# Kernel tuning notes

Measured on AMD Instinct MI355X. Metric: run time of the kernel, lower is better.

Reference implementation:

```python
import jax, jax.numpy as jnp
import numpy as np

N = 50000      # nodes
E = 800000     # edges (before self loops)
IN = 128       # in_channels
HID = 64       # hidden_channels
HEADS = 4      # num_heads
OUT = 40       # out_channels
NEG_SLOPE = 0.2


def setup_inputs() -> dict:
    key = jax.random.key(0)
    ks = jax.random.split(key, 16)
    x = jax.random.normal(ks[0], (N, IN), dtype=jnp.float32)
    edge_index = jax.random.randint(ks[1], (2, E), 0, N, dtype=jnp.int64)

    def lin(k, fan_in, fan_out):
        return jax.random.normal(k, (fan_in, fan_out), dtype=jnp.float32) * (1.0 / np.sqrt(fan_in))

    def att(k, h, c):
        return jax.random.normal(k, (h, c), dtype=jnp.float32) * (1.0 / np.sqrt(c))

    return {
        "x": x, "edge_index": edge_index,
        "W1": lin(ks[2], IN, HEADS * HID),
        "as1": att(ks[3], HEADS, HID), "ad1": att(ks[4], HEADS, HID),
        "b1": jnp.zeros((HEADS * HID,), jnp.float32),
        "W2": lin(ks[5], HEADS * HID, HEADS * HID),
        "as2": att(ks[6], HEADS, HID), "ad2": att(ks[7], HEADS, HID),
        "b2": jnp.zeros((HEADS * HID,), jnp.float32),
        "W3": lin(ks[8], HEADS * HID, OUT),
        "as3": att(ks[9], 1, OUT), "ad3": att(ks[10], 1, OUT),
        "b3": jnp.zeros((OUT,), jnp.float32),
    }


def _gat_layer(x, src, dst, W, a_src, a_dst, b):
    """One GATConv: linear -> per-edge attention -> segment softmax -> scatter-sum."""
    n = x.shape[0]
    H, C = a_src.shape
    h = (x @ W).reshape(n, H, C)                       # [N,H,C]
    al_s = jnp.einsum('nhc,hc->nh', h, a_src)          # [N,H]
    al_d = jnp.einsum('nhc,hc->nh', h, a_dst)          # [N,H]
    alpha = jax.nn.leaky_relu(al_s[src] + al_d[dst], NEG_SLOPE)  # [Etot,H]
    m = jax.ops.segment_max(alpha, dst, num_segments=n)          # stable softmax over incoming edges
    e = jnp.exp(alpha - m[dst])
    denom = jax.ops.segment_sum(e, dst, num_segments=n)
    attn = e / denom[dst]                              # [Etot,H]
    out = jax.ops.segment_sum(h[src] * attn[:, :, None], dst, num_segments=n)  # [N,H,C]
    return out.reshape(n, H * C) + b


def reference(x, edge_index, W1, as1, ad1, b1, W2, as2, ad2, b2, W3, as3, ad3, b3):
    # add self loops once (PyG GATConv default add_self_loops=True)
    loops = jnp.arange(N, dtype=edge_index.dtype)
    src = jnp.concatenate([edge_index[0], loops])
    dst = jnp.concatenate([edge_index[1], loops])

    h = _gat_layer(x, src, dst, W1, as1, ad1, b1)
    h = jax.nn.relu(h)                                 # dropout is identity in eval mode
    h = _gat_layer(h, src, dst, W2, as2, ad2, b2)
    h = jax.nn.relu(h)
    h = _gat_layer(h, src, dst, W3, as3, ad3, b3)      # final layer: 1 head
    return jax.nn.log_softmax(h, axis=-1)
```

## Files before the change

### kernel.cpp

```cpp
#include <hip/hip_runtime.h>
#include <math.h>

#define N_NODES 50000
#define N_EDGES 800000
#define ETOT    (N_EDGES + N_NODES)
#define EPAD_MAX 1200000
#define IN_CH   128
#define OUT_CH  40
#define NEG     0.2f
#define CAP     64

#define NPF   98
#define NFINE 512
#define FCAP  2400

typedef __attribute__((ext_vector_type(8))) short bf16x8;
typedef __attribute__((ext_vector_type(4))) float f32x4;
typedef __attribute__((ext_vector_type(2))) float f32x2;

__device__ inline unsigned short f2bf(float f) {
    unsigned int u = __float_as_uint(f);
    return (unsigned short)((u + 0x7FFFu + ((u >> 16) & 1u)) >> 16);
}
__device__ inline float bf2f(unsigned short u) {
    return __uint_as_float((unsigned int)u << 16);
}
__device__ inline float lrelu(float a) { return (a > 0.f) ? a : NEG * a; }

__global__ __launch_bounds__(256) void k_bkt(const int* __restrict__ ei,
                                             int* __restrict__ fcur,
                                             unsigned int* __restrict__ fbuf,
                                             const float* __restrict__ W1,
                                             const float* __restrict__ W2,
                                             const float* __restrict__ W3,
                                             unsigned short* __restrict__ Wt1,
                                             unsigned short* __restrict__ Wt2,
                                             unsigned short* __restrict__ Wt3) {
    if (blockIdx.x >= 256) {
        int i = (blockIdx.x - 256) * 256 + threadIdx.x;
        if (i < 32768) {
            int n = i >> 7, k = i & 127;
            Wt1[i] = f2bf(W1[(long)k * 256 + n]);
        } else if (i < 98304) {
            int j = i - 32768;
            int n = j >> 8, k = j & 255;
            Wt2[j] = f2bf(W2[(long)k * 256 + n]);
        } else if (i < 114688) {
            int j = i - 98304;
            int n = j >> 8, k = j & 255;
            Wt3[j] = (n < OUT_CH) ? f2bf(W3[(long)k * OUT_CH + n]) : (unsigned short)0;
        }
        return;
    }
    __shared__ int lcnt[NFINE], lbase[NFINE], lcur[NFINE];
    int tid = threadIdx.x;
    for (int i = tid; i < NFINE; i += 256) lcnt[i] = 0;
    __syncthreads();
    for (int i = blockIdx.x * 256 + tid; i < ETOT; i += 256 * 256) {
        int d = (i < N_EDGES) ? ei[N_EDGES + i] : (i - N_EDGES);
        atomicAdd(&lcnt[d / NPF], 1);
    }
    __syncthreads();
    for (int i = tid; i < NFINE; i += 256) {
        lbase[i] = atomicAdd(&fcur[i], lcnt[i]);
        lcur[i] = 0;
    }
    __syncthreads();
    for (int i = blockIdx.x * 256 + tid; i < ETOT; i += 256 * 256) {
        int s, d;
        if (i < N_EDGES) { s = ei[i]; d = ei[N_EDGES + i]; }
        else             { s = i - N_EDGES; d = s; }
        int p = d / NPF;
        int off = atomicAdd(&lcur[p], 1);
        fbuf[(long)p * FCAP + lbase[p] + off] = (unsigned int)s | ((unsigned int)d << 16);
    }
}

__global__ __launch_bounds__(256) void k_deg(const int* __restrict__ fcur,
                                             const unsigned int* __restrict__ fbuf,
                                             int* __restrict__ deg,
                                             int* __restrict__ psum) {
    __shared__ int cnt[NPF];
    __shared__ int tot;
    int f = blockIdx.x;
    int tid = threadIdx.x;
    int n0 = f * NPF;
    int nend = min(n0 + NPF, N_NODES);
    int nn = nend - n0;
    if (tid < NPF) cnt[tid] = 0;
    if (tid == 0) tot = 0;
    __syncthreads();
    int n = fcur[f];
    for (int i = tid; i < n; i += 256)
        atomicAdd(&cnt[(int)(fbuf[(long)f * FCAP + i] >> 16) - n0], 1);
    __syncthreads();
    if (tid < NPF && tid < nn) {
        deg[n0 + tid] = cnt[tid];
        atomicAdd(&tot, (cnt[tid] + 7) & ~7);
    }
    __syncthreads();
    if (tid == 0) psum[f] = tot;
}

__global__ __launch_bounds__(512) void k_pscan(int* __restrict__ psum) {
    __shared__ int sh[NFINE];
    int tid = threadIdx.x;
    int v = psum[tid];
    int x = v;
    sh[tid] = x;
    __syncthreads();
    #pragma unroll
    for (int off = 1; off < NFINE; off <<= 1) {
        int t = (tid >= off) ? sh[tid - off] : 0;
        __syncthreads();
        x += t;
        sh[tid] = x;
        __syncthreads();
    }
    psum[tid] = x - v;
}

__global__ __launch_bounds__(256) void k_scat(const int* __restrict__ fcur,
                                              const unsigned int* __restrict__ fbuf,
                                              const int* __restrict__ deg,
                                              const int* __restrict__ psum,
                                              int* __restrict__ start,
                                              int* __restrict__ eSrc) {
    __shared__ int sval[128];
    __shared__ int offs[NPF];
    __shared__ int base[NPF];
    int f = blockIdx.x;
    int tid = threadIdx.x;
    int n0 = f * NPF;
    int nend = min(n0 + NPF, N_NODES);
    int nn = nend - n0;
    int pbase = psum[f];

    int pd = 0;
    if (tid < 128) {
        pd = (tid < nn) ? ((deg[n0 + tid] + 7) & ~7) : 0;
        sval[tid] = pd;
    }
    __syncthreads();
    #pragma unroll
    for (int off = 1; off < 128; off <<= 1) {
        int t = 0;
        if (tid < 128 && tid >= off) t = sval[tid - off];
        __syncthreads();
        if (tid < 128) sval[tid] += t;
        __syncthreads();
    }
    if (tid < 128 && tid < nn) {
        int st = pbase + sval[tid] - pd;
        start[n0 + tid] = st;
        offs[tid] = st;
        base[tid] = st;
    }
    __syncthreads();

    int n = fcur[f];
    for (int i = tid; i < n; i += 256) {
        unsigned int u = fbuf[(long)f * FCAP + i];
        int d = (int)(u >> 16);
        int pos = atomicAdd(&offs[d - n0], 1);
        eSrc[pos] = (int)(u & 0xFFFFu);
    }
    __syncthreads();
    if (tid < NPF && tid < nn) {
        int endp = offs[tid];
        int dg = endp - base[tid];
        int stop = base[tid] + ((dg + 7) & ~7);
        for (int k2 = endp; k2 < stop; ++k2) eSrc[k2] = -1;
    }
}

#define PITCH 40
template<int BN, int FM, int FN, bool CVT, bool FP8OUT, bool L4>
__global__ __launch_bounds__(256) void k_mfma(const void* __restrict__ Araw,
                                              const unsigned short* __restrict__ Bt,
                                              void* __restrict__ Cout,
                                              const float* __restrict__ a_s,
                                              const float* __restrict__ a_d,
                                              float* __restrict__ als,
                                              float* __restrict__ ald,
                                              int M, int K, int Ncol) {
    __shared__ unsigned short As[128 * PITCH];
    __shared__ unsigned short Bs[BN * PITCH];
    const int WCOLS = BN / (FN * 16);
    int tid = threadIdx.x;
    int wave = tid >> 6, lane = tid & 63;
    int quad = lane >> 4, l16 = lane & 15;
    int wr = wave / WCOLS, wc = wave % WCOLS;
    long row0 = (long)blockIdx.x * 128;
    int col0 = blockIdx.y * BN;

    f32x4 acc[FM][FN] = {};

    for (int k0 = 0; k0 < K; k0 += 32) {
        for (int c = tid; c < 512; c += 256) {
            int r = c >> 2, kp = (c & 3) << 3;
            long gr = row0 + r;
            if (CVT) {
                const float* A32 = (const float*)Araw;
                ushort4 lo = {0,0,0,0}, hi = {0,0,0,0};
                if (gr < M) {
                    float4 v0 = *(const float4*)(A32 + gr * K + k0 + kp);
                    float4 v1 = *(const float4*)(A32 + gr * K + k0 + kp + 4);
                    lo.x = f2bf(v0.x); lo.y = f2bf(v0.y); lo.z = f2bf(v0.z); lo.w = f2bf(v0.w);
                    hi.x = f2bf(v1.x); hi.y = f2bf(v1.y); hi.z = f2bf(v1.z); hi.w = f2bf(v1.w);
                }
                *(ushort4*)(As + r * PITCH + kp) = lo;
                *(ushort4*)(As + r * PITCH + kp + 4) = hi;
            } else {
                const unsigned short* A16 = (const unsigned short*)Araw;
                uint4 v = {0u, 0u, 0u, 0u};
                if (gr < M) v = *(const uint4*)(A16 + gr * K + k0 + kp);
                *(uint4*)(As + r * PITCH + kp) = v;
            }
        }
        for (int c = tid; c < BN * 4; c += 256) {
            int r = c >> 2, kp = (c & 3) << 3;
            uint4 v = *(const uint4*)(Bt + (long)(col0 + r) * K + k0 + kp);
            *(uint4*)(Bs + r * PITCH + kp) = v;
        }
        __syncthreads();
        bf16x8 af[FM], bfr[FN];
        #pragma unroll
        for (int i = 0; i < FM; ++i)
            af[i] = *(const bf16x8*)(As + (wr * FM * 16 + i * 16 + l16) * PITCH + quad * 8);
        #pragma unroll
        for (int j = 0; j < FN; ++j)
            bfr[j] = *(const bf16x8*)(Bs + (wc * FN * 16 + j * 16 + l16) * PITCH + quad * 8);
        #pragma unroll
        for (int i = 0; i < FM; ++i)
            #pragma unroll
            for (int j = 0; j < FN; ++j)
                acc[i][j] = __builtin_amdgcn_mfma_f32_16x16x32_bf16(af[i], bfr[j], acc[i][j], 0, 0, 0);
        __syncthreads();
    }

    {
        int head = L4 ? (blockIdx.y * WCOLS + wc) : 0;
        float as_v[FN], ad_v[FN];
        #pragma unroll
        for (int j = 0; j < FN; ++j) {
            int cidx = j * 16 + l16;
            if (L4) {
                as_v[j] = a_s[head * 64 + cidx];
                ad_v[j] = a_d[head * 64 + cidx];
            } else {
                as_v[j] = (cidx < OUT_CH) ? a_s[cidx] : 0.f;
                ad_v[j] = (cidx < OUT_CH) ? a_d[cidx] : 0.f;
            }
        }
        #pragma unroll
        for (int i = 0; i < FM; ++i) {
            #pragma unroll
            for (int v = 0; v < 4; ++v) {
                float ps = acc[i][0][v] * as_v[0] + acc[i][1][v] * as_v[1]
                         + acc[i][2][v] * as_v[2] + acc[i][3][v] * as_v[3];
                float pd = acc[i][0][v] * ad_v[0] + acc[i][1][v] * ad_v[1]
                         + acc[i][2][v] * ad_v[2] + acc[i][3][v] * ad_v[3];
                #pragma unroll
                for (int off = 1; off < 16; off <<= 1) {
                    ps += __shfl_xor(ps, off);
                    pd += __shfl_xor(pd, off);
                }
                if (l16 == 0) {
                    long row = row0 + wr * (FM * 16) + i * 16 + quad * 4 + v;
                    if (row < M) {
                        if (L4) { als[row * 4 + head] = ps; ald[row * 4 + head] = pd; }
                        else    { als[row] = ps; ald[row] = pd; }
                    }
                }
            }
        }
    }

    if (FP8OUT) {
        unsigned char* C8 = (unsigned char*)Cout;
        #pragma unroll
        for (int i = 0; i < FM; ++i) {
            #pragma unroll
            for (int v = 0; v < 4; ++v) {
                long row = row0 + wr * FM * 16 + i * 16 + quad * 4 + v;
                if (row < M) {
                    int p01 = __builtin_amdgcn_cvt_pk_fp8_f32(acc[i][0][v], acc[i][1][v], 0, false);
                    int p23 = __builtin_amdgcn_cvt_pk_fp8_f32(acc[i][2][v], acc[i][3][v], 0, false);
                    unsigned char* b = C8 + row * 256 + col0 + wc * (FN * 16) + l16;
                    b[0]  = (unsigned char)(p01 & 0xFF);
                    b[16] = (unsigned char)((p01 >> 8) & 0xFF);
                    b[32] = (unsigned char)(p23 & 0xFF);
                    b[48] = (unsigned char)((p23 >> 8) & 0xFF);
                }
            }
        }
    } else {
        unsigned short* C = (unsigned short*)Cout;
        #pragma unroll
        for (int i = 0; i < FM; ++i) {
            long rowb = row0 + wr * FM * 16 + i * 16 + quad * 4;
            #pragma unroll
            for (int j = 0; j < FN; ++j) {
                int col = col0 + wc * FN * 16 + j * 16 + l16;
                if (col < Ncol) {
                    #pragma unroll
                    for (int v = 0; v < 4; ++v) {
                        long r = rowb + v;
                        if (r < M) C[r * Ncol + col] = f2bf(acc[i][j][v]);
                    }
                }
            }
        }
    }
}

__global__ __launch_bounds__(256) void k_agg4(const unsigned char* __restrict__ h8,
                                              const int* __restrict__ start,
                                              const int* __restrict__ deg,
                                              const int* __restrict__ eSrc,
                                              const float* __restrict__ als,
                                              const float* __restrict__ ald,
                                              const float* __restrict__ bias,
                                              unsigned short* __restrict__ out) {
    __shared__ float wbuf[4][CAP * 4];
    __shared__ int   sbuf[4][CAP];
    int wid = threadIdx.x >> 6;
    int node = (blockIdx.x * blockDim.x + threadIdx.x) >> 6;
    int lane = threadIdx.x & 63;
    if (node >= N_NODES) return;
    int st = start[node];
    int dgp = (deg[node] + 7) & ~7;
    const int* ep = eSrc + st;

    int l16 = lane & 15, headw = lane >> 4;
    float aldd4 = ald[node * 4 + headw];
    int ncap = (dgp < CAP) ? dgp : CAP;
    for (int c = 0; c < ncap; c += 16) {
        int slot = c + l16;
        bool ok = (slot < ncap);
        int raw = ok ? ep[slot] : -1;
        int ss = (raw < 0) ? 0 : raw;
        float a = als[(long)ss * 4 + headw] + aldd4;
        float w = (raw < 0) ? 0.f : __expf(lrelu(a));
        if (ok) {
            wbuf[wid][slot * 4 + headw] = w;
            if (headw == 0) sbuf[wid][slot] = ss;
        }
    }

    int half = lane >> 5;
    int hl = lane & 31;
    int head8 = hl >> 3;
    float den = 0.f;
    f32x2 acc2[4] = {};

    int ncpair = ncap >> 1;
    int jA = 0, jB = ncpair - 4;

    auto do_pairs = [&](int p0, int p1, int p2, int p3) {
        int slot[4] = {p0 * 2 + half, p1 * 2 + half, p2 * 2 + half, p3 * 2 + half};
        int s[4];
        float w[4];
        #pragma unroll
        for (int u = 0; u < 4; ++u) {
            s[u] = sbuf[wid][slot[u]];
            w[u] = wbuf[wid][slot[u] * 4 + head8];
        }
        uint2 hv[4];
        #pragma unroll
        for (int u = 0; u < 4; ++u)
            hv[u] = *(const uint2*)(h8 + (long)s[u] * 256 + hl * 8);
        #pragma unroll
        for (int u = 0; u < 4; ++u) {
            den += w[u];
            f32x2 w2; w2.x = w[u]; w2.y = w[u];
            acc2[0] += w2 * __builtin_amdgcn_cvt_pk_f32_fp8((int)hv[u].x, false);
            acc2[1] += w2 * __builtin_amdgcn_cvt_pk_f32_fp8((int)hv[u].x, true);
            acc2[2] += w2 * __builtin_amdgcn_cvt_pk_f32_fp8((int)hv[u].y, false);
            acc2[3] += w2 * __builtin_amdgcn_cvt_pk_f32_fp8((int)hv[u].y, true);
        }
    };

    while (jA < jB) {
        do_pairs(jA, jA + 1, jB, jB + 1);
        do_pairs(jA + 2, jA + 3, jB + 2, jB + 3);
        jA += 8; jB -= 8;
        jA -= 4; jB += 4;
    }
    if (jA == jB) {
        do_pairs(jA, jA + 1, jA + 2, jA + 3);
    }

    if (dgp > ncap) {
        float aldd8 = ald[node * 4 + head8];
        for (int j = ncap; j < dgp; j += 2) {
            int raw = ep[j + half];
            int ss = (raw < 0) ? 0 : raw;
            float w = (raw < 0) ? 0.f : __expf(lrelu(als[(long)ss * 4 + head8] + aldd8));
            uint2 hv = *(const uint2*)(h8 + (long)ss * 256 + hl * 8);
            den += w;
            f32x2 w2; w2.x = w; w2.y = w;
            acc2[0] += w2 * __builtin_amdgcn_cvt_pk_f32_fp8((int)hv.x, false);
            acc2[1] += w2 * __builtin_amdgcn_cvt_pk_f32_fp8((int)hv.x, true);
            acc2[2] += w2 * __builtin_amdgcn_cvt_pk_f32_fp8((int)hv.y, false);
            acc2[3] += w2 * __builtin_amdgcn_cvt_pk_f32_fp8((int)hv.y, true);
        }
    }

    den += __shfl_xor(den, 32);
    #pragma unroll
    for (int c = 0; c < 4; ++c) {
        acc2[c].x += __shfl_xor(acc2[c].x, 32);
        acc2[c].y += __shfl_xor(acc2[c].y, 32);
    }

    if (half == 0) {
        float inv = 1.f / den;
        int cb = hl * 8;
        float4 b0 = *(const float4*)(bias + cb);
        float4 b1 = *(const float4*)(bias + cb + 4);
        float v0 = fmaxf(acc2[0].x * inv + b0.x, 0.f);
        float v1 = fmaxf(acc2[0].y * inv + b0.y, 0.f);
        float v2 = fmaxf(acc2[1].x * inv + b0.z, 0.f);
        float v3 = fmaxf(acc2[1].y * inv + b0.w, 0.f);
        float v4 = fmaxf(acc2[2].x * inv + b1.x, 0.f);
        float v5 = fmaxf(acc2[2].y * inv + b1.y, 0.f);
        float v6 = fmaxf(acc2[3].x * inv + b1.z, 0.f);
        float v7 = fmaxf(acc2[3].y * inv + b1.w, 0.f);
        uint4 o;
        o.x = (unsigned int)f2bf(v0) | ((unsigned int)f2bf(v1) << 16);
        o.y = (unsigned int)f2bf(v2) | ((unsigned int)f2bf(v3) << 16);
        o.z = (unsigned int)f2bf(v4) | ((unsigned int)f2bf(v5) << 16);
        o.w = (unsigned int)f2bf(v6) | ((unsigned int)f2bf(v7) << 16);
        *(uint4*)(out + (long)node * 256 + cb) = o;
    }
}

__global__ __launch_bounds__(256) void k_agg1(const unsigned short* __restrict__ h,
                                              const int* __restrict__ start,
                                              const int* __restrict__ deg,
                                              const int* __restrict__ eSrc,
                                              const float* __restrict__ als,
                                              const float* __restrict__ ald,
                                              const float* __restrict__ bias,
                                              float* __restrict__ out) {
    int node = (blockIdx.x * blockDim.x + threadIdx.x) >> 6;
    int lane = threadIdx.x & 63;
    if (node >= N_NODES) return;
    int q = lane >> 4, r = lane & 15;
    bool act = (r < 10);
    int st = start[node];
    int dgp = (deg[node] + 7) & ~7;
    const int* ep = eSrc + st;
    float aldd = ald[node];

    float den = 0.f;
    float4 acc = {0.f, 0.f, 0.f, 0.f};

    int j = 0;
    for (; j + 16 <= dgp; j += 16) {
        int base = j + q * 4;
        int s[4];
        float w[4];
        #pragma unroll
        for (int u = 0; u < 4; ++u) s[u] = ep[base + u];
        #pragma unroll
        for (int u = 0; u < 4; ++u) {
            int raw = s[u];
            int ss = (raw < 0) ? 0 : raw;
            w[u] = (raw < 0) ? 0.f : __expf(lrelu(als[ss] + aldd));
            s[u] = ss;
        }
        ushort4 hh[4];
        #pragma unroll
        for (int u = 0; u < 4; ++u) {
            ushort4 t = {0, 0, 0, 0};
            if (act) t = *(const ushort4*)(h + (long)s[u] * OUT_CH + r * 4);
            hh[u] = t;
        }
        #pragma unroll
        for (int u = 0; u < 4; ++u) {
            den += w[u];
            acc.x += w[u] * bf2f(hh[u].x);
            acc.y += w[u] * bf2f(hh[u].y);
            acc.z += w[u] * bf2f(hh[u].z);
            acc.w += w[u] * bf2f(hh[u].w);
        }
    }
    if (j < dgp) {
        int base = j + q * 2;
        int s[2];
        float w[2];
        #pragma unroll
        for (int u = 0; u < 2; ++u) s[u] = ep[base + u];
        #pragma unroll
        for (int u = 0; u < 2; ++u) {
            int raw = s[u];
            int ss = (raw < 0) ? 0 : raw;
            w[u] = (raw < 0) ? 0.f : __expf(lrelu(als[ss] + aldd));
            s[u] = ss;
        }
        ushort4 hh[2];
        #pragma unroll
        for (int u = 0; u < 2; ++u) {
            ushort4 t = {0, 0, 0, 0};
            if (act) t = *(const ushort4*)(h + (long)s[u] * OUT_CH + r * 4);
            hh[u] = t;
        }
        #pragma unroll
        for (int u = 0; u < 2; ++u) {
            den += w[u];
            acc.x += w[u] * bf2f(hh[u].x);
            acc.y += w[u] * bf2f(hh[u].y);
            acc.z += w[u] * bf2f(hh[u].z);
            acc.w += w[u] * bf2f(hh[u].w);
        }
    }

    #pragma unroll
    for (int off = 16; off < 64; off <<= 1) {
        acc.x += __shfl_xor(acc.x, off);
        acc.y += __shfl_xor(acc.y, off);
        acc.z += __shfl_xor(acc.z, off);
        acc.w += __shfl_xor(acc.w, off);
        den   += __shfl_xor(den, off);
    }
    float inv = 1.f / den;
    float4 bv = {0.f, 0.f, 0.f, 0.f};
    if (act) bv = *(const float4*)(bias + r * 4);
    float4 v;
    v.x = acc.x * inv + bv.x;
    v.y = acc.y * inv + bv.y;
    v.z = acc.z * inv + bv.z;
    v.w = acc.w * inv + bv.w;
    float mx = act ? fmaxf(fmaxf(v.x, v.y), fmaxf(v.z, v.w)) : -INFINITY;
    #pragma unroll
    for (int off = 1; off < 16; off <<= 1) mx = fmaxf(mx, __shfl_xor(mx, off));
    float sum = act ? (__expf(v.x - mx) + __expf(v.y - mx) + __expf(v.z - mx) + __expf(v.w - mx)) : 0.f;
    #pragma unroll
    for (int off = 1; off < 16; off <<= 1) sum += __shfl_xor(sum, off);
    float lse = mx + logf(sum);
    if (q == 0 && act) {
        float4 o;
        o.x = v.x - lse;
        o.y = v.y - lse;
        o.z = v.z - lse;
        o.w = v.w - lse;
        *(float4*)(out + (long)node * OUT_CH + r * 4) = o;
    }
}

extern "C" void kernel_launch(void* const* d_in, const int* in_sizes, int n_in,
                              void* d_out, int out_size, void* d_ws, size_t ws_size,
                              hipStream_t stream) {
    (void)in_sizes; (void)n_in; (void)out_size; (void)ws_size;
    const float* x   = (const float*)d_in[0];
    const int*   ei  = (const int*)d_in[1];
    const float* W1  = (const float*)d_in[2];
    const float* as1 = (const float*)d_in[3];
    const float* ad1 = (const float*)d_in[4];
    const float* b1  = (const float*)d_in[5];
    const float* W2  = (const float*)d_in[6];
    const float* as2 = (const float*)d_in[7];
    const float* ad2 = (const float*)d_in[8];
    const float* b2  = (const float*)d_in[9];
    const float* W3  = (const float*)d_in[10];
    const float* as3 = (const float*)d_in[11];
    const float* ad3 = (const float*)d_in[12];
    const float* b3  = (const float*)d_in[13];
    float* out = (float*)d_out;

    char* p = (char*)d_ws;
    auto alloc = [&](size_t b) { char* r = p; p += (b + 255) & ~(size_t)255; return r; };
    int*   deg   = (int*)alloc((size_t)N_NODES * 4);
    int*   start = (int*)alloc((size_t)N_NODES * 4);
    int*   psum  = (int*)alloc((size_t)NFINE * 4);
    int*   fcur  = (int*)alloc((size_t)NFINE * 4);
    unsigned int* fbuf = (unsigned int*)alloc((size_t)NFINE * FCAP * 4);
    int*   eSrc  = (int*)alloc((size_t)EPAD_MAX * 4);
    float* als   = (float*)alloc((size_t)N_NODES * 4 * 4);
    float* ald   = (float*)alloc((size_t)N_NODES * 4 * 4);
    unsigned char*  hA8  = (unsigned char*)alloc((size_t)N_NODES * 256);
    unsigned short* hBbf = (unsigned short*)alloc((size_t)N_NODES * 256 * 2);
    unsigned short* h3bf = (unsigned short*)alloc((size_t)N_NODES * OUT_CH * 2);
    unsigned short* Wt1  = (unsigned short*)alloc((size_t)256 * IN_CH * 2);
    unsigned short* Wt2  = (unsigned short*)alloc((size_t)256 * 256 * 2);
    unsigned short* Wt3  = (unsigned short*)alloc((size_t)64 * 256 * 2);

    const int WB = (N_NODES + 3) / 4;
    const int MB = (N_NODES + 127) / 128;

    hipMemsetAsync(fcur, 0, (size_t)NFINE * 4, stream);
    k_bkt<<<256 + 448, 256, 0, stream>>>(ei, fcur, fbuf, W1, W2, W3, Wt1, Wt2, Wt3);
    k_deg<<<NFINE, 256, 0, stream>>>(fcur, fbuf, deg, psum);
    k_pscan<<<1, NFINE, 0, stream>>>(psum);
    k_scat<<<NFINE, 256, 0, stream>>>(fcur, fbuf, deg, psum, start, eSrc);

    k_mfma<128, 4, 4, true, true, true><<<dim3(MB, 2), 256, 0, stream>>>(
        x, Wt1, hA8, as1, ad1, als, ald, N_NODES, IN_CH, 256);
    k_agg4<<<WB, 256, 0, stream>>>(hA8, start, deg, eSrc, als, ald, b1, hBbf);

    k_mfma<128, 4, 4, false, true, true><<<dim3(MB, 2), 256, 0, stream>>>(
        hBbf, Wt2, hA8, as2, ad2, als, ald, N_NODES, 256, 256);
    k_agg4<<<WB, 256, 0, stream>>>(hA8, start, deg, eSrc, als, ald, b2, hBbf);

    k_mfma<64, 2, 4, false, false, false><<<dim3(MB, 1), 256, 0, stream>>>(
        hBbf, Wt3, h3bf, as3, ad3, als, ald, N_NODES, 256, OUT_CH);
    k_agg1<<<WB, 256, 0, stream>>>(h3bf, start, deg, eSrc, als, ald, b3, out);
}
```

Measured before the change: 314.1 us.

## Fuse CSR build into one kernel, pad to 4, pipeline agg4 gathers

Merges the degree, prefix-scan and scatter kernels into a single k_build. Each block now claims its output range with an atomicAdd on a global cursor instead of a separate scan pass, which removes two launches and a round trip through global memory. Edge padding per node drops from multiples of 8 to multiples of 4, so fewer dummy edges are processed. k_agg4 packs the source offset and the weight into one shared-memory uint2 and double-buffers the gather loads to overlap them with the FMAs. The cursor memset relies on psum and fcur being allocated next to each other, and the CSR segments are no longer laid out in node order.

```diff
diff --git a/kernel.cpp b/kernel.cpp
--- a/kernel.cpp
+++ b/kernel.cpp
@@ -76,69 +76,31 @@
     }
 }
 
-__global__ __launch_bounds__(256) void k_deg(const int* __restrict__ fcur,
-                                             const unsigned int* __restrict__ fbuf,
-                                             int* __restrict__ deg,
-                                             int* __restrict__ psum) {
+__global__ __launch_bounds__(256) void k_build(const int* __restrict__ fcur,
+                                               const unsigned int* __restrict__ fbuf,
+                                               int* __restrict__ deg,
+                                               int* __restrict__ gcur,
+                                               int* __restrict__ start,
+                                               int* __restrict__ eSrc) {
     __shared__ int cnt[NPF];
-    __shared__ int tot;
+    __shared__ int sval[128];
+    __shared__ int offs[NPF];
+    __shared__ int base_[NPF];
+    __shared__ int pbase;
     int f = blockIdx.x;
     int tid = threadIdx.x;
     int n0 = f * NPF;
     int nend = min(n0 + NPF, N_NODES);
     int nn = nend - n0;
     if (tid < NPF) cnt[tid] = 0;
-    if (tid == 0) tot = 0;
     __syncthreads();
     int n = fcur[f];
     for (int i = tid; i < n; i += 256)
         atomicAdd(&cnt[(int)(fbuf[(long)f * FCAP + i] >> 16) - n0], 1);
     __syncthreads();
-    if (tid < NPF && tid < nn) {
-        deg[n0 + tid] = cnt[tid];
-        atomicAdd(&tot, (cnt[tid] + 7) & ~7);
-    }
-    __syncthreads();
-    if (tid == 0) psum[f] = tot;
-}
-
-__global__ __launch_bounds__(512) void k_pscan(int* __restrict__ psum) {
-    __shared__ int sh[NFINE];
-    int tid = threadIdx.x;
-    int v = psum[tid];
-    int x = v;
-    sh[tid] = x;
-    __syncthreads();
-    #pragma unroll
-    for (int off = 1; off < NFINE; off <<= 1) {
-        int t = (tid >= off) ? sh[tid - off] : 0;
-        __syncthreads();
-        x += t;
-        sh[tid] = x;
-        __syncthreads();
-    }
-    psum[tid] = x - v;
-}
-
-__global__ __launch_bounds__(256) void k_scat(const int* __restrict__ fcur,
-                                              const unsigned int* __restrict__ fbuf,
-                                              const int* __restrict__ deg,
-                                              const int* __restrict__ psum,
-                                              int* __restrict__ start,
-                                              int* __restrict__ eSrc) {
-    __shared__ int sval[128];
-    __shared__ int offs[NPF];
-    __shared__ int base[NPF];
-    int f = blockIdx.x;
-    int tid = threadIdx.x;
-    int n0 = f * NPF;
-    int nend = min(n0 + NPF, N_NODES);
-    int nn = nend - n0;
-    int pbase = psum[f];
-
     int pd = 0;
     if (tid < 128) {
-        pd = (tid < nn) ? ((deg[n0 + tid] + 7) & ~7) : 0;
+        pd = (tid < nn) ? ((cnt[tid] + 3) & ~3) : 0;
         sval[tid] = pd;
     }
     __syncthreads();
@@ -150,15 +112,16 @@
         if (tid < 128) sval[tid] += t;
         __syncthreads();
     }
-    if (tid < 128 && tid < nn) {
+    if (tid == 0) pbase = atomicAdd(gcur, sval[127]);
+    __syncthreads();
+    if (tid < nn) {
         int st = pbase + sval[tid] - pd;
+        deg[n0 + tid] = cnt[tid];
         start[n0 + tid] = st;
         offs[tid] = st;
-        base[tid] = st;
-    }
-    __syncthreads();
-
-    int n = fcur[f];
+        base_[tid] = st;
+    }
+    __syncthreads();
     for (int i = tid; i < n; i += 256) {
         unsigned int u = fbuf[(long)f * FCAP + i];
         int d = (int)(u >> 16);
@@ -166,10 +129,10 @@
         eSrc[pos] = (int)(u & 0xFFFFu);
     }
     __syncthreads();
-    if (tid < NPF && tid < nn) {
+    if (tid < nn) {
         int endp = offs[tid];
-        int dg = endp - base[tid];
-        int stop = base[tid] + ((dg + 7) & ~7);
+        int dg = endp - base_[tid];
+        int stop = base_[tid] + ((dg + 3) & ~3);
         for (int k2 = endp; k2 < stop; ++k2) eSrc[k2] = -1;
     }
 }
@@ -323,14 +286,13 @@
                                               const float* __restrict__ ald,
                                               const float* __restrict__ bias,
                                               unsigned short* __restrict__ out) {
-    __shared__ float wbuf[4][CAP * 4];
-    __shared__ int   sbuf[4][CAP];
+    __shared__ uint2 swbuf[4][CAP * 4];
     int wid = threadIdx.x >> 6;
     int node = (blockIdx.x * blockDim.x + threadIdx.x) >> 6;
     int lane = threadIdx.x & 63;
     if (node >= N_NODES) return;
     int st = start[node];
-    int dgp = (deg[node] + 7) & ~7;
+    int dgp = (deg[node] + 3) & ~3;
     const int* ep = eSrc + st;
 
     int l16 = lane & 15, headw = lane >> 4;
@@ -344,33 +306,33 @@
         float a = als[(long)ss * 4 + headw] + aldd4;
         float w = (raw < 0) ? 0.f : __expf(lrelu(a));
         if (ok) {
-            wbuf[wid][slot * 4 + headw] = w;
-            if (headw == 0) sbuf[wid][slot] = ss;
+            uint2 t;
+            t.x = (unsigned int)(ss << 8);
+            t.y = __float_as_uint(w);
+            swbuf[wid][slot * 4 + headw] = t;
         }
     }
 
     int half = lane >> 5;
     int hl = lane & 31;
     int head8 = hl >> 3;
+    int hlOff = hl * 8;
     float den = 0.f;
     f32x2 acc2[4] = {};
 
-    int ncpair = ncap >> 1;
-    int jA = 0, jB = ncpair - 4;
-
-    auto do_pairs = [&](int p0, int p1, int p2, int p3) {
-        int slot[4] = {p0 * 2 + half, p1 * 2 + half, p2 * 2 + half, p3 * 2 + half};
-        int s[4];
-        float w[4];
+    float wA[4], wB[4];
+    uint2 hA[4], hB[4];
+
+    auto ldstage = [&](int r, float* w, uint2* hv) {
+        int b = r * 8 + half * 4;
         #pragma unroll
         for (int u = 0; u < 4; ++u) {
-            s[u] = sbuf[wid][slot[u]];
-            w[u] = wbuf[wid][slot[u] * 4 + head8];
-        }
-        uint2 hv[4];
-        #pragma unroll
-        for (int u = 0; u < 4; ++u)
-            hv[u] = *(const uint2*)(h8 + (long)s[u] * 256 + hl * 8);
+            uint2 t = swbuf[wid][(b + u) * 4 + head8];
+            w[u] = __uint_as_float(t.y);
+            hv[u] = *(const uint2*)(h8 + (long)t.x + hlOff);
+        }
+    };
+    auto consume = [&](float* w, uint2* hv) {
         #pragma unroll
         for (int u = 0; u < 4; ++u) {
             den += w[u];
@@ -382,14 +344,33 @@
         }
     };
 
-    while (jA < jB) {
-        do_pairs(jA, jA + 1, jB, jB + 1);
-        do_pairs(jA + 2, jA + 3, jB + 2, jB + 3);
-        jA += 8; jB -= 8;
-        jA -= 4; jB += 4;
-    }
-    if (jA == jB) {
-        do_pairs(jA, jA + 1, jA + 2, jA + 3);
+    int nr = ncap >> 3;
+    if (nr > 0) {
+        ldstage(0, wA, hA);
+        int r = 1;
+        for (; r + 1 < nr; r += 2) {
+            ldstage(r, wB, hB);
+            consume(wA, hA);
+            ldstage(r + 1, wA, hA);
+            consume(wB, hB);
+        }
+        if (r < nr) { ldstage(r, wB, hB); consume(wA, hA); consume(wB, hB); }
+        else        { consume(wA, hA); }
+    }
+    if (ncap & 4) {
+        int b = (ncap - 4) + half * 2;
+        #pragma unroll
+        for (int u = 0; u < 2; ++u) {
+            uint2 t = swbuf[wid][(b + u) * 4 + head8];
+            float w = __uint_as_float(t.y);
+            uint2 hv = *(const uint2*)(h8 + (long)t.x + hlOff);
+            den += w;
+            f32x2 w2; w2.x = w; w2.y = w;
+            acc2[0] += w2 * __builtin_amdgcn_cvt_pk_f32_fp8((int)hv.x, false);
+            acc2[1] += w2 * __builtin_amdgcn_cvt_pk_f32_fp8((int)hv.x, true);
+            acc2[2] += w2 * __builtin_amdgcn_cvt_pk_f32_fp8((int)hv.y, false);
+            acc2[3] += w2 * __builtin_amdgcn_cvt_pk_f32_fp8((int)hv.y, true);
+        }
     }
 
     if (dgp > ncap) {
@@ -451,7 +432,7 @@
     int q = lane >> 4, r = lane & 15;
     bool act = (r < 10);
     int st = start[node];
-    int dgp = (deg[node] + 7) & ~7;
+    int dgp = (deg[node] + 3) & ~3;
     const int* ep = eSrc + st;
     float aldd = ald[node];
 
@@ -488,34 +469,17 @@
             acc.w += w[u] * bf2f(hh[u].w);
         }
     }
-    if (j < dgp) {
-        int base = j + q * 2;
-        int s[2];
-        float w[2];
-        #pragma unroll
-        for (int u = 0; u < 2; ++u) s[u] = ep[base + u];
-        #pragma unroll
-        for (int u = 0; u < 2; ++u) {
-            int raw = s[u];
-            int ss = (raw < 0) ? 0 : raw;
-            w[u] = (raw < 0) ? 0.f : __expf(lrelu(als[ss] + aldd));
-            s[u] = ss;
-        }
-        ushort4 hh[2];
-        #pragma unroll
-        for (int u = 0; u < 2; ++u) {
-            ushort4 t = {0, 0, 0, 0};
-            if (act) t = *(const ushort4*)(h + (long)s[u] * OUT_CH + r * 4);
-            hh[u] = t;
-        }
-        #pragma unroll
-        for (int u = 0; u < 2; ++u) {
-            den += w[u];
-            acc.x += w[u] * bf2f(hh[u].x);
-            acc.y += w[u] * bf2f(hh[u].y);
-            acc.z += w[u] * bf2f(hh[u].z);
-            acc.w += w[u] * bf2f(hh[u].w);
-        }
+    for (; j < dgp; j += 4) {
+        int raw = ep[j + q];
+        int ss = (raw < 0) ? 0 : raw;
+        float w = (raw < 0) ? 0.f : __expf(lrelu(als[ss] + aldd));
+        ushort4 t = {0, 0, 0, 0};
+        if (act) t = *(const ushort4*)(h + (long)ss * OUT_CH + r * 4);
+        den += w;
+        acc.x += w * bf2f(t.x);
+        acc.y += w * bf2f(t.y);
+        acc.z += w * bf2f(t.z);
+        acc.w += w * bf2f(t.w);
     }
 
     #pragma unroll
@@ -591,11 +555,9 @@
     const int WB = (N_NODES + 3) / 4;
     const int MB = (N_NODES + 127) / 128;
 
-    hipMemsetAsync(fcur, 0, (size_t)NFINE * 4, stream);
+    hipMemsetAsync(psum, 0, (size_t)NFINE * 8, stream);
     k_bkt<<<256 + 448, 256, 0, stream>>>(ei, fcur, fbuf, W1, W2, W3, Wt1, Wt2, Wt3);
-    k_deg<<<NFINE, 256, 0, stream>>>(fcur, fbuf, deg, psum);
-    k_pscan<<<1, NFINE, 0, stream>>>(psum);
-    k_scat<<<NFINE, 256, 0, stream>>>(fcur, fbuf, deg, psum, start, eSrc);
+    k_build<<<NFINE, 256, 0, stream>>>(fcur, fbuf, deg, psum, start, eSrc);
 
     k_mfma<128, 4, 4, true, true, true><<<dim3(MB, 2), 256, 0, stream>>>(
         x, Wt1, hA8, as1, ad1, als, ald, N_NODES, IN_CH, 256);
```

Measured after the change: 322.8 us. +2.8%, slower.
